# Kernel tuning notes

Measured on AMD Instinct MI355X. Metric: run time of the kernel, lower is better.

Reference implementation:

```python
import jax, jax.numpy as jnp
import numpy as np

B, N, DIM, HEAD = 32, 1024, 512, 8
W_SP = 32  # sqrt(N), query spatial side
SCALE = DIM ** (-0.5)  # original uses full dim, not head_dim
EPS = 1e-5


def setup_inputs() -> dict:
    key = jax.random.key(0)
    ks = jax.random.split(key, 7)
    feats = jax.random.normal(ks[0], (B, N, DIM), dtype=jnp.float32)
    W_q = jax.random.normal(ks[1], (DIM, DIM), dtype=jnp.float32) * (DIM ** -0.5)
    conv_w = jax.random.normal(ks[2], (2 * DIM, DIM, 3, 3), dtype=jnp.float32) * ((DIM * 9) ** -0.5)
    conv_b = jnp.zeros((2 * DIM,), dtype=jnp.float32)
    ln_gamma = jnp.ones((2 * DIM,), dtype=jnp.float32)
    ln_beta = jnp.zeros((2 * DIM,), dtype=jnp.float32)
    W_out = jax.random.normal(ks[3], (DIM, DIM), dtype=jnp.float32) * (DIM ** -0.5)
    return {"feats": feats, "W_q": W_q, "conv_w": conv_w, "conv_b": conv_b,
            "ln_gamma": ln_gamma, "ln_beta": ln_beta, "W_out": W_out}


def reference(feats, W_q, conv_w, conv_b, ln_gamma, ln_beta, W_out):
    b, n, dim = feats.shape
    h = HEAD
    d = dim // h
    # trans_kv: 'b (w h) c -> b c w h' -> conv2d(dim->2dim, k3 s2 p1) -> 'b c w h -> b (w h) c' -> LN
    x = feats.reshape(b, W_SP, W_SP, dim).transpose(0, 3, 1, 2)  # NCHW
    kv = jax.lax.conv_general_dilated(
        x, conv_w, window_strides=(2, 2), padding=((1, 1), (1, 1)),
        dimension_numbers=("NCHW", "OIHW", "NCHW"))
    kv = kv + conv_b[None, :, None, None]          # [b, 2dim, w2, w2]
    m = kv.shape[2] * kv.shape[3]
    kv = kv.reshape(b, 2 * dim, m).transpose(0, 2, 1)  # [b, m, 2dim]
    mu = jnp.mean(kv, axis=-1, keepdims=True)
    var = jnp.var(kv, axis=-1, keepdims=True)
    kv = (kv - mu) * jax.lax.rsqrt(var + EPS) * ln_gamma + ln_beta
    k, v = jnp.split(kv, 2, axis=-1)               # each [b, m, dim]
    q = feats @ W_q.T                               # [b, n, dim]
    q = q.reshape(b, n, h, d)
    k = k.reshape(b, m, h, d)
    v = v.reshape(b, m, h, d)
    alpha = jnp.einsum("bihd,bjhd->bhij", q, k) * SCALE  # [b, h, n, m]
    # NOTE: original computes Conv(alpha) into att, then overwrites with softmax(alpha);
    # the Conv block is dead code w.r.t. the output.
    att = jax.nn.softmax(alpha, axis=-1)
    out = jnp.einsum("bhij,bjhd->bhid", att, v)    # [b, h, n, d]
    out = out.transpose(0, 2, 1, 3).reshape(b, n, dim)
    out = out @ W_out.T                             # fc_out linear (dropout=identity in eval)
    return out
```

## Files before the change

### kernel.cpp

```cpp
#include <hip/hip_runtime.h>
#include <hip/hip_bf16.h>
#include <math.h>

#define B_    32
#define N_    1024
#define DIM_  512
#define HEAD_ 8
#define HD_   64
#define WSP   32
#define M2    256
#define CDIM  1024
#define KCONV 4608
#define KHALF 2304
#define EPS_  1e-5f
#define SCALE_ 0.044194173824159216f
#define PW    34

typedef __attribute__((ext_vector_type(8))) short bf16x8;
typedef __attribute__((ext_vector_type(4))) float f32x4_t;
typedef const __attribute__((address_space(1))) void gas_t;
typedef __attribute__((address_space(3))) void las_t;

__device__ __forceinline__ ushort f2b(float x) {
  __hip_bfloat16 h = __float2bfloat16(x);
  return *reinterpret_cast<const ushort*>(&h);
}

__global__ __launch_bounds__(256) void misc_prep_kernel(
    ushort* __restrict__ featsp, const float* __restrict__ W_q,
    ushort* __restrict__ wqb, const float* __restrict__ W_out,
    ushort* __restrict__ woutb) {
  int blk = blockIdx.x;
  if (blk < 1056) {
    int t = blk * 256 + threadIdx.x;
    int b = t / 8448, r = t - b * 8448;
    int cell = r >> 6, ic8 = (r & 63) * 8;
    int iw, ih;
    if (cell < 34)      { iw = 0;  ih = cell; }
    else if (cell < 68) { iw = 33; ih = cell - 34; }
    else { int e = cell - 68; iw = 1 + (e >> 1); ih = (e & 1) * 33; }
    bf16x8 z = {};
    *reinterpret_cast<bf16x8*>(&featsp[(((size_t)b * PW + iw) * PW + ih) * 512 + ic8]) = z;
  } else if (blk < 1312) {
    int i = (blk - 1056) * 256 + threadIdx.x;
    float4 v = reinterpret_cast<const float4*>(W_q)[i];
    ushort4 o;
    o.x = f2b(v.x); o.y = f2b(v.y); o.z = f2b(v.z); o.w = f2b(v.w);
    reinterpret_cast<ushort4*>(wqb)[i] = o;
  } else {
    int i = (blk - 1312) * 256 + threadIdx.x;
    float4 v = reinterpret_cast<const float4*>(W_out)[i];
    ushort4 o;
    o.x = f2b(v.x); o.y = f2b(v.y); o.z = f2b(v.z); o.w = f2b(v.w);
    reinterpret_cast<ushort4*>(woutb)[i] = o;
  }
}

__global__ __launch_bounds__(256) void cast_featsp_kernel(
    const float* __restrict__ feats, ushort* __restrict__ featsp) {
  int i = blockIdx.x * 256 + threadIdx.x;
  int e = i * 4;
  int b = e >> 19, r = e & 524287;
  int n = r >> 9, ic = r & 511;
  int iw = n >> 5, ih = n & 31;
  float4 v = reinterpret_cast<const float4*>(feats)[i];
  ushort4 o;
  o.x = f2b(v.x); o.y = f2b(v.y); o.z = f2b(v.z); o.w = f2b(v.w);
  size_t dst = (((size_t)b * PW + iw + 1) * PW + ih + 1) * 512 + ic;
  *reinterpret_cast<ushort4*>(&featsp[dst]) = o;
}

__global__ __launch_bounds__(256) void permute_convw_kernel(
    const float* __restrict__ in, ushort* __restrict__ out) {
  int oc = blockIdx.y;
  int idx = blockIdx.x * 256 + threadIdx.x;
  int tap = idx >> 9, ic = idx & 511;
  out[(size_t)oc * KCONV + idx] = f2b(in[(size_t)oc * KCONV + ic * 9 + tap]);
}

__global__ __launch_bounds__(512, 2) void conv256_kernel(
    const ushort* __restrict__ featsp, const ushort* __restrict__ convwb,
    const float* __restrict__ conv_b, float* __restrict__ kvf,
    float* __restrict__ kvp1) {
  __shared__ __align__(16) ushort lds[2][32768];
  const int tid = threadIdx.x;
  const int lane = tid & 63, wid = tid >> 6;
  const int wr = wid >> 2, wc = wid & 3;
  const int lrow = lane & 15, lk = lane >> 4;
  const int kz = blockIdx.z;
  const int koff = kz * KHALF;

  const int l = blockIdx.y * gridDim.x + blockIdx.x;
  const int v = (l & 7) * 16 + (l >> 3);
  const int bm = (v >> 2) * 256;
  const int bn = (v & 3) * 256;
  const int bimg = bm >> 8;

  f32x4_t acc[8][4] = {};

  auto stage = [&](int buf, int kt) {
    int k0 = koff + (kt << 6);
#pragma unroll
    for (int i = 0; i < 4; ++i) {
      int s = i * 512 + tid;
      int row = s >> 3, ch = s & 7;
      int cl = ch ^ (row & 7);
      int kk = k0 + cl * 8;
      int tap = kk >> 9, ic = kk & 511;
      int kh = tap / 3, kw = tap - 3 * kh;
      int w2 = row >> 4, h2 = row & 15;
      const ushort* ga = &featsp[(((size_t)bimg * PW + 2 * w2 + kh) * PW + 2 * h2 + kw) * 512 + ic];
      __builtin_amdgcn_global_load_lds((gas_t*)ga,
          (las_t*)(&lds[buf][0] + (size_t)s * 8), 16, 0, 0);
    }
#pragma unroll
    for (int i = 0; i < 4; ++i) {
      int s = i * 512 + tid;
      int row = s >> 3, ch = s & 7;
      int cl = ch ^ (row & 7);
      const ushort* gb = &convwb[(size_t)(bn + row) * KCONV + k0 + cl * 8];
      __builtin_amdgcn_global_load_lds((gas_t*)gb,
          (las_t*)(&lds[buf][16384] + (size_t)s * 8), 16, 0, 0);
    }
  };

  const int NT = KHALF >> 6;
  stage(0, 0);
  for (int kt = 0; kt < NT; ++kt) {
    int cur = kt & 1;
    if (kt + 1 < NT) {
      stage(cur ^ 1, kt + 1);
      asm volatile("s_waitcnt vmcnt(8)" ::: "memory");
    } else {
      asm volatile("s_waitcnt vmcnt(0)" ::: "memory");
    }
    __builtin_amdgcn_s_barrier();
    __builtin_amdgcn_sched_barrier(0);
#pragma unroll
    for (int kk = 0; kk < 2; ++kk) {
      bf16x8 aF[8], bF[4];
#pragma unroll
      for (int m = 0; m < 8; ++m) {
        int row = wr * 128 + m * 16 + lrow;
        int ch = (kk * 4 + lk) ^ (row & 7);
        aF[m] = *reinterpret_cast<const bf16x8*>(&lds[cur][row * 64 + ch * 8]);
      }
#pragma unroll
      for (int n = 0; n < 4; ++n) {
        int row = wc * 64 + n * 16 + lrow;
        int ch = (kk * 4 + lk) ^ (row & 7);
        bF[n] = *reinterpret_cast<const bf16x8*>(&lds[cur][16384 + row * 64 + ch * 8]);
      }
#pragma unroll
      for (int m = 0; m < 8; ++m)
#pragma unroll
        for (int n = 0; n < 4; ++n)
          acc[m][n] = __builtin_amdgcn_mfma_f32_16x16x32_bf16(
              aF[m], bF[n], acc[m][n], 0, 0, 0);
    }
    __builtin_amdgcn_sched_barrier(0);
    __builtin_amdgcn_s_barrier();
  }

  float* Co = kz ? kvp1 : kvf;
#pragma unroll
  for (int m = 0; m < 8; ++m) {
#pragma unroll
    for (int n = 0; n < 4; ++n) {
      int col = bn + wc * 64 + n * 16 + lrow;
#pragma unroll
      for (int r = 0; r < 4; ++r) {
        int row = bm + wr * 128 + m * 16 + lk * 4 + r;
        float v2 = acc[m][n][r];
        if (kz == 0) v2 += conv_b[col];
        Co[(size_t)row * CDIM + col] = v2;
      }
    }
  }
}

template<int MODE>
__device__ __forceinline__ void gemm_body(
    ushort (*As)[128][32], ushort (*Bs)[128][32],
    int l, int nbn, int nwg,
    const ushort* __restrict__ A, const ushort* __restrict__ featsp,
    const ushort* __restrict__ Bw, float* __restrict__ Cf,
    ushort* __restrict__ Cb, int M, int N, int K) {
  const int tid = threadIdx.x;
  const int lane = tid & 63, wid = tid >> 6;
  const int wr = wid >> 1, wc = wid & 1;
  const int v = (l & 7) * (nwg >> 3) + (l >> 3);
  const int bm = (v / nbn) * 128, bn = (v % nbn) * 128;
  const int lrow = lane & 15, lk = lane >> 4;
  const int swz = (lrow >> 1) & 3;

  f32x4_t acc[4][4] = {};

  auto stage = [&](int buf, int kt) {
    int k0 = kt << 5;
#pragma unroll
    for (int it = 0; it < 2; ++it) {
      int idx = it * 256 + tid;
      int row = idx >> 2;
      int c = (((idx & 3) ^ ((idx >> 3) & 3))) * 8;
      const ushort* ga;
      if (MODE == 0) {
        ga = &A[(size_t)(bm + row) * K + k0 + c];
      } else {
        int p = bm + row;
        int b = p >> 10, n = p & 1023;
        int iw = n >> 5, ih = n & 31;
        ga = &featsp[(((size_t)b * PW + iw + 1) * PW + ih + 1) * 512 + k0 + c];
      }
      __builtin_amdgcn_global_load_lds((gas_t*)ga,
          (las_t*)(&As[buf][0][0] + (size_t)idx * 8), 16, 0, 0);
      const ushort* gb = &Bw[(size_t)(bn + row) * K + k0 + c];
      __builtin_amdgcn_global_load_lds((gas_t*)gb,
          (las_t*)(&Bs[buf][0][0] + (size_t)idx * 8), 16, 0, 0);
    }
  };

  stage(0, 0);
  const int NT = K >> 5;
  for (int kt = 0; kt < NT; ++kt) {
    int cur = kt & 1;
    if (kt + 1 < NT) {
      stage(cur ^ 1, kt + 1);
      asm volatile("s_waitcnt vmcnt(4)" ::: "memory");
    } else {
      asm volatile("s_waitcnt vmcnt(0)" ::: "memory");
    }
    __builtin_amdgcn_s_barrier();
    __builtin_amdgcn_sched_barrier(0);
    bf16x8 aF[4], bF[4];
#pragma unroll
    for (int m = 0; m < 4; ++m)
      aF[m] = *reinterpret_cast<const bf16x8*>(
          &As[cur][wr * 64 + m * 16 + lrow][(lk ^ swz) * 8]);
#pragma unroll
    for (int n = 0; n < 4; ++n)
      bF[n] = *reinterpret_cast<const bf16x8*>(
          &Bs[cur][wc * 64 + n * 16 + lrow][(lk ^ swz) * 8]);
#pragma unroll
    for (int m = 0; m < 4; ++m)
#pragma unroll
      for (int n = 0; n < 4; ++n)
        acc[m][n] = __builtin_amdgcn_mfma_f32_16x16x32_bf16(
            aF[m], bF[n], acc[m][n], 0, 0, 0);
    __builtin_amdgcn_sched_barrier(0);
    __builtin_amdgcn_s_barrier();
  }

#pragma unroll
  for (int m = 0; m < 4; ++m) {
#pragma unroll
    for (int n = 0; n < 4; ++n) {
      int col = bn + wc * 64 + n * 16 + lrow;
#pragma unroll
      for (int r = 0; r < 4; ++r) {
        int row = bm + wr * 64 + m * 16 + lk * 4 + r;
        float v2 = acc[m][n][r];
        if (MODE == 1) Cb[(size_t)row * N + col] = f2b(v2);
        else Cf[(size_t)row * N + col] = v2;
      }
    }
  }
}

__global__ __launch_bounds__(256) void qproj_kernel(
    const ushort* __restrict__ featsp, const ushort* __restrict__ wqb,
    ushort* __restrict__ qb) {
  __shared__ ushort As[2][128][32];
  __shared__ ushort Bs[2][128][32];
  int l = blockIdx.y * gridDim.x + blockIdx.x;
  gemm_body<1>(As, Bs, l, gridDim.x, gridDim.x * gridDim.y,
               nullptr, featsp, wqb, nullptr, qb, B_ * N_, DIM_, DIM_);
}

__global__ __launch_bounds__(256) void gemm0_kernel(
    const ushort* __restrict__ A, const ushort* __restrict__ Bw,
    float* __restrict__ Cf, int M, int N, int K) {
  __shared__ ushort As[2][128][32];
  __shared__ ushort Bs[2][128][32];
  int l = blockIdx.y * gridDim.x + blockIdx.x;
  gemm_body<0>(As, Bs, l, gridDim.x, gridDim.x * gridDim.y,
               A, nullptr, Bw, Cf, nullptr, M, N, K);
}

__global__ __launch_bounds__(256) void ln_kernel(
    const float* __restrict__ kvp0, const float* __restrict__ kvp1,
    const float* __restrict__ gamma, const float* __restrict__ beta,
    ushort* __restrict__ Kb, ushort* __restrict__ Vt) {
  const int p = blockIdx.x, tid = threadIdx.x;
  float4 a = reinterpret_cast<const float4*>(kvp0 + (size_t)p * CDIM)[tid];
  float4 b4 = reinterpret_cast<const float4*>(kvp1 + (size_t)p * CDIM)[tid];
  float4 x = make_float4(a.x + b4.x, a.y + b4.y, a.z + b4.z, a.w + b4.w);
  float s = x.x + x.y + x.z + x.w;
  float ss = x.x * x.x + x.y * x.y + x.z * x.z + x.w * x.w;
#pragma unroll
  for (int off = 32; off > 0; off >>= 1) {
    s += __shfl_down(s, off);
    ss += __shfl_down(ss, off);
  }
  __shared__ float sb[4], ssb[4];
  if ((tid & 63) == 0) { sb[tid >> 6] = s; ssb[tid >> 6] = ss; }
  __syncthreads();
  float tot = sb[0] + sb[1] + sb[2] + sb[3];
  float tot2 = ssb[0] + ssb[1] + ssb[2] + ssb[3];
  float mu = tot * (1.f / CDIM);
  float var = tot2 * (1.f / CDIM) - mu * mu;
  float rstd = rsqrtf(var + EPS_);
  float4 g = reinterpret_cast<const float4*>(gamma)[tid];
  float4 bb = reinterpret_cast<const float4*>(beta)[tid];
  ushort o0 = f2b((x.x - mu) * rstd * g.x + bb.x);
  ushort o1 = f2b((x.y - mu) * rstd * g.y + bb.y);
  ushort o2 = f2b((x.z - mu) * rstd * g.z + bb.z);
  ushort o3 = f2b((x.w - mu) * rstd * g.w + bb.w);
  int b = p >> 8, j = p & 255;
  int c = tid * 4;
  if (c < DIM_) {
    int h = c >> 6, d = c & 63;
    ushort4 o = make_ushort4(o0, o1, o2, o3);
    *reinterpret_cast<ushort4*>(&Kb[(((size_t)(b * 8 + h)) * M2 + j) * HD_ + d]) = o;
  } else {
    int c2 = c - DIM_;
    int h = c2 >> 6, d = c2 & 63;
    size_t base = ((size_t)(b * 8 + h) * HD_ + d) * M2 + j;
    Vt[base]           = o0;
    Vt[base + M2]      = o1;
    Vt[base + 2 * M2]  = o2;
    Vt[base + 3 * M2]  = o3;
  }
}

__global__ __launch_bounds__(512, 2) void attn_mfma_kernel(
    const ushort* __restrict__ qb, const ushort* __restrict__ Kb,
    const ushort* __restrict__ Vt, ushort* __restrict__ attob) {
  __shared__ __align__(16) char lds[131072];
  char* lp = lds;
  const int tid = threadIdx.x;
  const int lane = tid & 63, wid = tid >> 6;
  const int lr = lane & 15, lk = lane >> 4;
  const int bh = blockIdx.x;
  const int b = bh >> 3, h = bh & 7;

  auto ks_byte = [](int j, int d) -> int {
    return (j << 7) + (((d << 1)) ^ ((j & 7) << 4));
  };
  auto vt_byte = [](int d, int j) -> int {
    return 32768 + (d << 9) + (((j << 1)) ^ ((d & 7) << 4));
  };
  auto p_byte = [](int w, int q4, int kv) -> int {
    return 65536 + (w << 13) + (q4 << 9) + (((kv << 1)) ^ ((q4 & 7) << 4));
  };

  const ushort* Khead  = Kb + (size_t)bh * M2 * HD_;
  const ushort* Vthead = Vt + (size_t)bh * HD_ * M2;

#pragma unroll
  for (int it = 0; it < 4; ++it) {
    int o = (it * 512 + tid) * 16;
    int j = o >> 7, c = (o >> 4) & 7;
    int cl = c ^ (j & 7);
    __builtin_amdgcn_global_load_lds((gas_t*)(Khead + j * HD_ + cl * 8),
        (las_t*)(lp + o), 16, 0, 0);
  }
#pragma unroll
  for (int it = 0; it < 4; ++it) {
    int o = (it * 512 + tid) * 16;
    int d = o >> 9, c = (o >> 4) & 31;
    int cl = c ^ (d & 7);
    __builtin_amdgcn_global_load_lds((gas_t*)(Vthead + d * M2 + cl * 8),
        (las_t*)(lp + 32768 + o), 16, 0, 0);
  }

  __syncthreads();

  for (int qp = 0; qp < 4; ++qp) {
    const int qbase = qp * 256 + wid * 32;
    bf16x8 qf[2][2];
#pragma unroll
    for (int mf = 0; mf < 2; ++mf)
#pragma unroll
      for (int ks = 0; ks < 2; ++ks)
        qf[mf][ks] = *reinterpret_cast<const bf16x8*>(
            qb + ((size_t)(b * N_ + qbase + mf * 16 + lr)) * DIM_ + h * HD_ + ks * 32 + lk * 8);

    f32x4_t sacc[2][16] = {};
    __builtin_amdgcn_s_setprio(1);
#pragma unroll
    for (int ks = 0; ks < 2; ++ks) {
#pragma unroll
      for (int nj = 0; nj < 16; ++nj) {
        bf16x8 kf = *reinterpret_cast<const bf16x8*>(
            lp + ks_byte(nj * 16 + lr, ks * 32 + lk * 8));
        sacc[0][nj] = __builtin_amdgcn_mfma_f32_16x16x32_bf16(qf[0][ks], kf, sacc[0][nj], 0, 0, 0);
        sacc[1][nj] = __builtin_amdgcn_mfma_f32_16x16x32_bf16(qf[1][ks], kf, sacc[1][nj], 0, 0, 0);
      }
    }
    __builtin_amdgcn_s_setprio(0);

    float linv[2][4];
    f32x4_t oacc[2][4] = {};
#pragma unroll
    for (int mf = 0; mf < 2; ++mf) {
#pragma unroll
      for (int r = 0; r < 4; ++r) {
        float pv[16];
        float sum = 0.f;
#pragma unroll
        for (int nj = 0; nj < 16; ++nj) {
          pv[nj] = __expf(sacc[mf][nj][r] * SCALE_);
          sum += pv[nj];
        }
        sum += __shfl_xor(sum, 1);
        sum += __shfl_xor(sum, 2);
        sum += __shfl_xor(sum, 4);
        sum += __shfl_xor(sum, 8);
        linv[mf][r] = 1.f / sum;
        int q4 = lk * 4 + r;
#pragma unroll
        for (int nj = 0; nj < 16; ++nj)
          *reinterpret_cast<ushort*>(lp + p_byte(wid, q4, nj * 16 + lr)) = f2b(pv[nj]);
      }
      __builtin_amdgcn_s_setprio(1);
#pragma unroll
      for (int ks2 = 0; ks2 < 8; ++ks2) {
        bf16x8 pf = *reinterpret_cast<const bf16x8*>(
            lp + p_byte(wid, lr, ks2 * 32 + lk * 8));
#pragma unroll
        for (int df = 0; df < 4; ++df) {
          bf16x8 vf = *reinterpret_cast<const bf16x8*>(
              lp + vt_byte(df * 16 + lr, ks2 * 32 + lk * 8));
          oacc[mf][df] = __builtin_amdgcn_mfma_f32_16x16x32_bf16(pf, vf, oacc[mf][df], 0, 0, 0);
        }
      }
      __builtin_amdgcn_s_setprio(0);
    }

#pragma unroll
    for (int mf = 0; mf < 2; ++mf)
#pragma unroll
      for (int df = 0; df < 4; ++df)
#pragma unroll
        for (int r = 0; r < 4; ++r) {
          int qrow = qbase + mf * 16 + lk * 4 + r;
          int dcol = df * 16 + lr;
          float val = oacc[mf][df][r] * linv[mf][r];
          attob[((size_t)(b * N_ + qrow)) * DIM_ + h * HD_ + dcol] = f2b(val);
        }
  }
}

extern "C" void kernel_launch(void* const* d_in, const int* in_sizes, int n_in,
                              void* d_out, int out_size, void* d_ws, size_t ws_size,
                              hipStream_t stream) {
  const float* feats  = (const float*)d_in[0];
  const float* W_q    = (const float*)d_in[1];
  const float* conv_w = (const float*)d_in[2];
  const float* conv_b = (const float*)d_in[3];
  const float* ln_g   = (const float*)d_in[4];
  const float* ln_b   = (const float*)d_in[5];
  const float* W_out  = (const float*)d_in[6];
  float* out = (float*)d_out;

  const size_t FP_ELEMS = (size_t)B_ * PW * PW * DIM_;
  char* ws = (char*)d_ws;
  ushort* featsp = (ushort*)ws;  ws += FP_ELEMS * 2;
  ushort* qb     = (ushort*)ws;  ws += (size_t)B_ * N_ * DIM_ * 2;
  ushort* attob  = (ushort*)ws;  ws += (size_t)B_ * N_ * DIM_ * 2;
  float*  kvf    = (float*)ws;   ws += (size_t)B_ * M2 * CDIM * 4;
  ushort* convwb = (ushort*)ws;  ws += (size_t)CDIM * KCONV * 2;
  ushort* wqb    = (ushort*)ws;  ws += (size_t)DIM_ * DIM_ * 2;
  ushort* woutb  = (ushort*)ws;  ws += (size_t)DIM_ * DIM_ * 2;
  ushort* Kb     = (ushort*)ws;  ws += (size_t)B_ * HEAD_ * M2 * HD_ * 2;
  ushort* Vt     = (ushort*)ws;  ws += (size_t)B_ * HEAD_ * M2 * HD_ * 2;
  float* kvp1 = (float*)attob;

  misc_prep_kernel<<<1568, 256, 0, stream>>>(featsp, W_q, wqb, W_out, woutb);
  cast_featsp_kernel<<<16384, 256, 0, stream>>>(feats, featsp);
  permute_convw_kernel<<<dim3(18, CDIM), 256, 0, stream>>>(conv_w, convwb);

  qproj_kernel<<<dim3(DIM_ / 128, (B_ * N_) / 128), 256, 0, stream>>>(
      featsp, wqb, qb);

  conv256_kernel<<<dim3(CDIM / 256, (B_ * M2) / 256, 2), 512, 0, stream>>>(
      featsp, convwb, conv_b, kvf, kvp1);

  ln_kernel<<<B_ * M2, 256, 0, stream>>>(kvf, kvp1, ln_g, ln_b, Kb, Vt);

  attn_mfma_kernel<<<B_ * HEAD_, 512, 0, stream>>>(qb, Kb, Vt, attob);

  gemm0_kernel<<<dim3(DIM_ / 128, (B_ * N_) / 128), 256, 0, stream>>>(
      attob, woutb, out, B_ * N_, DIM_, DIM_);
}
```

Before: 259.9 us.

## Restructure conv GEMM mainloop into 4-slot K=32 pipeline with interleaved loads

Replaces the double-buffered K=64 LDS pipeline in the conv implicit GEMM with four K=32 slots kept three stages ahead. Global-to-LDS loads are split into four chunks and interleaved with MFMA sub-phases, and s_setprio is raised around the MFMA bursts. The goal is to hide global-load latency better and to overlap LDS reads with matrix math. In exchange it adds more barriers per K-step and halves the MFMA work between barriers, which could cost more in synchronisation than it saves.

```diff
diff --git a/kernel.cpp b/kernel.cpp
--- a/kernel.cpp
+++ b/kernel.cpp
@@ -82,7 +82,7 @@
     const ushort* __restrict__ featsp, const ushort* __restrict__ convwb,
     const float* __restrict__ conv_b, float* __restrict__ kvf,
     float* __restrict__ kvp1) {
-  __shared__ __align__(16) ushort lds[2][32768];
+  __shared__ __align__(16) ushort lds[4][16384];
   const int tid = threadIdx.x;
   const int lane = tid & 63, wid = tid >> 6;
   const int wr = wid >> 2, wc = wid & 3;
@@ -98,67 +98,81 @@
 
   f32x4_t acc[8][4] = {};
 
-  auto stage = [&](int buf, int kt) {
-    int k0 = koff + (kt << 6);
-#pragma unroll
-    for (int i = 0; i < 4; ++i) {
-      int s = i * 512 + tid;
-      int row = s >> 3, ch = s & 7;
-      int cl = ch ^ (row & 7);
-      int kk = k0 + cl * 8;
-      int tap = kk >> 9, ic = kk & 511;
+  auto stage1 = [&](int hh, int j) {
+    int slot = hh & 3;
+    int kbase = koff + hh * 32;
+    if (j < 2) {
+      int s = j * 512 + tid;
+      int q = s >> 3, e = s & 7;
+      int el = e ^ (q & 7);
+      int r = q * 2 + (el >> 2);
+      int c = el & 3;
+      int kk2 = kbase + c * 8;
+      int tap = kk2 >> 9, ic = kk2 & 511;
       int kh = tap / 3, kw = tap - 3 * kh;
-      int w2 = row >> 4, h2 = row & 15;
+      int w2 = r >> 4, h2 = r & 15;
       const ushort* ga = &featsp[(((size_t)bimg * PW + 2 * w2 + kh) * PW + 2 * h2 + kw) * 512 + ic];
       __builtin_amdgcn_global_load_lds((gas_t*)ga,
-          (las_t*)(&lds[buf][0] + (size_t)s * 8), 16, 0, 0);
-    }
-#pragma unroll
-    for (int i = 0; i < 4; ++i) {
-      int s = i * 512 + tid;
-      int row = s >> 3, ch = s & 7;
-      int cl = ch ^ (row & 7);
-      const ushort* gb = &convwb[(size_t)(bn + row) * KCONV + k0 + cl * 8];
+          (las_t*)(&lds[slot][0] + (size_t)s * 8), 16, 0, 0);
+    } else {
+      int s = (j - 2) * 512 + tid;
+      int q = s >> 3, e = s & 7;
+      int el = e ^ (q & 7);
+      int r = q * 2 + (el >> 2);
+      int c = el & 3;
+      const ushort* gb = &convwb[(size_t)(bn + r) * KCONV + kbase + c * 8];
       __builtin_amdgcn_global_load_lds((gas_t*)gb,
-          (las_t*)(&lds[buf][16384] + (size_t)s * 8), 16, 0, 0);
-    }
-  };
-
-  const int NT = KHALF >> 6;
-  stage(0, 0);
-  for (int kt = 0; kt < NT; ++kt) {
-    int cur = kt & 1;
-    if (kt + 1 < NT) {
-      stage(cur ^ 1, kt + 1);
-      asm volatile("s_waitcnt vmcnt(8)" ::: "memory");
-    } else {
-      asm volatile("s_waitcnt vmcnt(0)" ::: "memory");
-    }
-    __builtin_amdgcn_s_barrier();
-    __builtin_amdgcn_sched_barrier(0);
-#pragma unroll
-    for (int kk = 0; kk < 2; ++kk) {
-      bf16x8 aF[8], bF[4];
-#pragma unroll
-      for (int m = 0; m < 8; ++m) {
-        int row = wr * 128 + m * 16 + lrow;
-        int ch = (kk * 4 + lk) ^ (row & 7);
-        aF[m] = *reinterpret_cast<const bf16x8*>(&lds[cur][row * 64 + ch * 8]);
-      }
+          (las_t*)(&lds[slot][8192] + (size_t)s * 8), 16, 0, 0);
+    }
+  };
+
+  auto rdA = [&](int slot, int mf) -> bf16x8 {
+    int r = wr * 128 + mf * 16 + lrow;
+    int q = r >> 1, o = r & 1;
+    int e = (o * 4 + lk) ^ (q & 7);
+    return *reinterpret_cast<const bf16x8*>(&lds[slot][q * 64 + e * 8]);
+  };
+  auto rdB = [&](int slot, int nf) -> bf16x8 {
+    int r = wc * 64 + nf * 16 + lrow;
+    int q = r >> 1, o = r & 1;
+    int e = (o * 4 + lk) ^ (q & 7);
+    return *reinterpret_cast<const bf16x8*>(&lds[slot][8192 + q * 64 + e * 8]);
+  };
+
+  const int H = KHALF / 32;
+#pragma unroll
+  for (int hh = 0; hh < 3; ++hh)
+#pragma unroll
+    for (int j = 0; j < 4; ++j) stage1(hh, j);
+  asm volatile("s_waitcnt vmcnt(8)" ::: "memory");
+  __builtin_amdgcn_s_barrier();
+
+  for (int h = 0; h < H; ++h) {
+    int slot = h & 3;
+    bf16x8 bF[4];
+#pragma unroll
+    for (int p = 0; p < 4; ++p) {
+      if (p == 0) {
+        bF[0] = rdB(slot, 0); bF[1] = rdB(slot, 1);
+        bF[2] = rdB(slot, 2); bF[3] = rdB(slot, 3);
+      }
+      bf16x8 aa0 = rdA(slot, 2 * p), aa1 = rdA(slot, 2 * p + 1);
+      if (h + 3 < H) stage1(h + 3, p);
+      __builtin_amdgcn_s_barrier();
+      asm volatile("s_waitcnt lgkmcnt(0)" ::: "memory");
+      __builtin_amdgcn_sched_barrier(0);
+      __builtin_amdgcn_s_setprio(1);
 #pragma unroll
       for (int n = 0; n < 4; ++n) {
-        int row = wc * 64 + n * 16 + lrow;
-        int ch = (kk * 4 + lk) ^ (row & 7);
-        bF[n] = *reinterpret_cast<const bf16x8*>(&lds[cur][16384 + row * 64 + ch * 8]);
-      }
-#pragma unroll
-      for (int m = 0; m < 8; ++m)
-#pragma unroll
-        for (int n = 0; n < 4; ++n)
-          acc[m][n] = __builtin_amdgcn_mfma_f32_16x16x32_bf16(
-              aF[m], bF[n], acc[m][n], 0, 0, 0);
-    }
-    __builtin_amdgcn_sched_barrier(0);
+        acc[2 * p][n]     = __builtin_amdgcn_mfma_f32_16x16x32_bf16(aa0, bF[n], acc[2 * p][n], 0, 0, 0);
+        acc[2 * p + 1][n] = __builtin_amdgcn_mfma_f32_16x16x32_bf16(aa1, bF[n], acc[2 * p + 1][n], 0, 0, 0);
+      }
+      __builtin_amdgcn_s_setprio(0);
+      if (p < 3) __builtin_amdgcn_s_barrier();
+    }
+    if (h <= H - 4)      asm volatile("s_waitcnt vmcnt(8)" ::: "memory");
+    else if (h == H - 3) asm volatile("s_waitcnt vmcnt(4)" ::: "memory");
+    else                 asm volatile("s_waitcnt vmcnt(0)" ::: "memory");
     __builtin_amdgcn_s_barrier();
   }
 
```

New measurement: 261.1 us. Within noise of the previous version (+0.5%).

## Merge prep kernels into one launch and transpose V via LDS

Applied to the files above, without the earlier changes.

Folds the three preprocessing kernels (padding zero-fill, weight casts, conv weight permute, feats cast) into a single launch to cut launch overhead. The LayerNorm kernel now writes V in row layout with a vector store instead of four scattered 2-byte stores. A new small kernel then transposes V into the layout the attention kernel expects, staging through shared memory. Vb reuses the conv weight buffer, which is dead by then. This adds one more launch and an extra pass over V in exchange for coalesced writes.

```diff
diff --git a/kernel.cpp b/kernel.cpp
--- a/kernel.cpp
+++ b/kernel.cpp
@@ -26,10 +26,11 @@
   return *reinterpret_cast<const ushort*>(&h);
 }
 
-__global__ __launch_bounds__(256) void misc_prep_kernel(
-    ushort* __restrict__ featsp, const float* __restrict__ W_q,
-    ushort* __restrict__ wqb, const float* __restrict__ W_out,
-    ushort* __restrict__ woutb) {
+__global__ __launch_bounds__(256) void prep_kernel(
+    const float* __restrict__ feats, ushort* __restrict__ featsp,
+    const float* __restrict__ W_q, ushort* __restrict__ wqb,
+    const float* __restrict__ W_out, ushort* __restrict__ woutb,
+    const float* __restrict__ conv_w, ushort* __restrict__ convwb) {
   int blk = blockIdx.x;
   if (blk < 1056) {
     int t = blk * 256 + threadIdx.x;
@@ -47,35 +48,30 @@
     ushort4 o;
     o.x = f2b(v.x); o.y = f2b(v.y); o.z = f2b(v.z); o.w = f2b(v.w);
     reinterpret_cast<ushort4*>(wqb)[i] = o;
-  } else {
+  } else if (blk < 1568) {
     int i = (blk - 1312) * 256 + threadIdx.x;
     float4 v = reinterpret_cast<const float4*>(W_out)[i];
     ushort4 o;
     o.x = f2b(v.x); o.y = f2b(v.y); o.z = f2b(v.z); o.w = f2b(v.w);
     reinterpret_cast<ushort4*>(woutb)[i] = o;
-  }
-}
-
-__global__ __launch_bounds__(256) void cast_featsp_kernel(
-    const float* __restrict__ feats, ushort* __restrict__ featsp) {
-  int i = blockIdx.x * 256 + threadIdx.x;
-  int e = i * 4;
-  int b = e >> 19, r = e & 524287;
-  int n = r >> 9, ic = r & 511;
-  int iw = n >> 5, ih = n & 31;
-  float4 v = reinterpret_cast<const float4*>(feats)[i];
-  ushort4 o;
-  o.x = f2b(v.x); o.y = f2b(v.y); o.z = f2b(v.z); o.w = f2b(v.w);
-  size_t dst = (((size_t)b * PW + iw + 1) * PW + ih + 1) * 512 + ic;
-  *reinterpret_cast<ushort4*>(&featsp[dst]) = o;
-}
-
-__global__ __launch_bounds__(256) void permute_convw_kernel(
-    const float* __restrict__ in, ushort* __restrict__ out) {
-  int oc = blockIdx.y;
-  int idx = blockIdx.x * 256 + threadIdx.x;
-  int tap = idx >> 9, ic = idx & 511;
-  out[(size_t)oc * KCONV + idx] = f2b(in[(size_t)oc * KCONV + ic * 9 + tap]);
+  } else if (blk < 20000) {
+    int t2 = blk - 1568;
+    int oc = t2 / 18, sub = t2 - oc * 18;
+    int idx = sub * 256 + threadIdx.x;
+    int tap = idx >> 9, ic = idx & 511;
+    convwb[(size_t)oc * KCONV + idx] = f2b(conv_w[(size_t)oc * KCONV + ic * 9 + tap]);
+  } else {
+    int i = (blk - 20000) * 256 + threadIdx.x;
+    int e = i * 4;
+    int b = e >> 19, r = e & 524287;
+    int n = r >> 9, ic = r & 511;
+    int iw = n >> 5, ih = n & 31;
+    float4 v = reinterpret_cast<const float4*>(feats)[i];
+    ushort4 o;
+    o.x = f2b(v.x); o.y = f2b(v.y); o.z = f2b(v.z); o.w = f2b(v.w);
+    size_t dst = (((size_t)b * PW + iw + 1) * PW + ih + 1) * 512 + ic;
+    *reinterpret_cast<ushort4*>(&featsp[dst]) = o;
+  }
 }
 
 __global__ __launch_bounds__(512, 2) void conv256_kernel(
@@ -290,7 +286,7 @@
 __global__ __launch_bounds__(256) void ln_kernel(
     const float* __restrict__ kvp0, const float* __restrict__ kvp1,
     const float* __restrict__ gamma, const float* __restrict__ beta,
-    ushort* __restrict__ Kb, ushort* __restrict__ Vt) {
+    ushort* __restrict__ Kb, ushort* __restrict__ Vb) {
   const int p = blockIdx.x, tid = threadIdx.x;
   float4 a = reinterpret_cast<const float4*>(kvp0 + (size_t)p * CDIM)[tid];
   float4 b4 = reinterpret_cast<const float4*>(kvp1 + (size_t)p * CDIM)[tid];
@@ -312,24 +308,49 @@
   float rstd = rsqrtf(var + EPS_);
   float4 g = reinterpret_cast<const float4*>(gamma)[tid];
   float4 bb = reinterpret_cast<const float4*>(beta)[tid];
-  ushort o0 = f2b((x.x - mu) * rstd * g.x + bb.x);
-  ushort o1 = f2b((x.y - mu) * rstd * g.y + bb.y);
-  ushort o2 = f2b((x.z - mu) * rstd * g.z + bb.z);
-  ushort o3 = f2b((x.w - mu) * rstd * g.w + bb.w);
+  ushort4 o;
+  o.x = f2b((x.x - mu) * rstd * g.x + bb.x);
+  o.y = f2b((x.y - mu) * rstd * g.y + bb.y);
+  o.z = f2b((x.z - mu) * rstd * g.z + bb.z);
+  o.w = f2b((x.w - mu) * rstd * g.w + bb.w);
   int b = p >> 8, j = p & 255;
   int c = tid * 4;
   if (c < DIM_) {
     int h = c >> 6, d = c & 63;
-    ushort4 o = make_ushort4(o0, o1, o2, o3);
     *reinterpret_cast<ushort4*>(&Kb[(((size_t)(b * 8 + h)) * M2 + j) * HD_ + d]) = o;
   } else {
     int c2 = c - DIM_;
     int h = c2 >> 6, d = c2 & 63;
-    size_t base = ((size_t)(b * 8 + h) * HD_ + d) * M2 + j;
-    Vt[base]           = o0;
-    Vt[base + M2]      = o1;
-    Vt[base + 2 * M2]  = o2;
-    Vt[base + 3 * M2]  = o3;
+    *reinterpret_cast<ushort4*>(&Vb[(((size_t)(b * 8 + h)) * M2 + j) * HD_ + d]) = o;
+  }
+}
+
+__global__ __launch_bounds__(256) void vtrans_kernel(
+    const ushort* __restrict__ Vb, ushort* __restrict__ Vt) {
+  __shared__ ushort t[64][65];
+  const int bh = blockIdx.x, tid = threadIdx.x;
+  const ushort* src = Vb + (size_t)bh * M2 * HD_;
+  ushort* dst = Vt + (size_t)bh * HD_ * M2;
+  for (int j0 = 0; j0 < M2; j0 += 64) {
+    __syncthreads();
+#pragma unroll
+    for (int it = 0; it < 2; ++it) {
+      int s = it * 256 + tid;
+      int j = s >> 3, d0 = (s & 7) * 8;
+      bf16x8 v = *reinterpret_cast<const bf16x8*>(src + (size_t)(j0 + j) * HD_ + d0);
+#pragma unroll
+      for (int e = 0; e < 8; ++e) t[d0 + e][j] = (ushort)v[e];
+    }
+    __syncthreads();
+#pragma unroll
+    for (int it = 0; it < 2; ++it) {
+      int s = it * 256 + tid;
+      int d = s >> 3, jj0 = (s & 7) * 8;
+      bf16x8 o;
+#pragma unroll
+      for (int e = 0; e < 8; ++e) o[e] = (short)t[d][jj0 + e];
+      *reinterpret_cast<bf16x8*>(dst + (size_t)d * M2 + j0 + jj0) = o;
+    }
   }
 }
 
@@ -476,10 +497,10 @@
   ushort* Kb     = (ushort*)ws;  ws += (size_t)B_ * HEAD_ * M2 * HD_ * 2;
   ushort* Vt     = (ushort*)ws;  ws += (size_t)B_ * HEAD_ * M2 * HD_ * 2;
   float* kvp1 = (float*)attob;
-
-  misc_prep_kernel<<<1568, 256, 0, stream>>>(featsp, W_q, wqb, W_out, woutb);
-  cast_featsp_kernel<<<16384, 256, 0, stream>>>(feats, featsp);
-  permute_convw_kernel<<<dim3(18, CDIM), 256, 0, stream>>>(conv_w, convwb);
+  ushort* Vb = convwb;
+
+  prep_kernel<<<36384, 256, 0, stream>>>(
+      feats, featsp, W_q, wqb, W_out, woutb, conv_w, convwb);
 
   qproj_kernel<<<dim3(DIM_ / 128, (B_ * N_) / 128), 256, 0, stream>>>(
       featsp, wqb, qb);
@@ -487,7 +508,9 @@
   conv256_kernel<<<dim3(CDIM / 256, (B_ * M2) / 256, 2), 512, 0, stream>>>(
       featsp, convwb, conv_b, kvf, kvp1);
 
-  ln_kernel<<<B_ * M2, 256, 0, stream>>>(kvf, kvp1, ln_g, ln_b, Kb, Vt);
+  ln_kernel<<<B_ * M2, 256, 0, stream>>>(kvf, kvp1, ln_g, ln_b, Kb, Vb);
+
+  vtrans_kernel<<<B_ * HEAD_, 256, 0, stream>>>(Vb, Vt);
 
   attn_mfma_kernel<<<B_ * HEAD_, 512, 0, stream>>>(qb, Kb, Vt, attob);
 
```

Result: faster. 242.7 us (-6.6%).
